# Performance work log

Hardware: AMD Instinct MI355X
Metric: run time of the kernel (lower is better)

Reference implementation:

```python
import jax, jax.numpy as jnp
import numpy as np

PD_THR = 1e-6  # positive-definiteness floor for the diagonal covariance

N_IN, DIM, BATCH = 8192, 128, 4096


def setup_inputs() -> dict:
    key = jax.random.key(0)
    kx, km = jax.random.split(key)
    x = jax.random.normal(kx, (BATCH, DIM), dtype=jnp.float32)
    mean = jax.random.normal(km, (N_IN, DIM), dtype=jnp.float32)
    diag = jnp.ones((N_IN, DIM), dtype=jnp.float32)
    return {"x": x, "mean": mean, "diag": diag}


def reference(x, mean, diag):
    """Energies[b, i] = KL( N(x_b, I) || N(mean_i, diag(diag_i)) ).

    Diagonal-Gaussian KL:
      0.5 * sum_d [ log(diag_id) + (1 + (x_bd - mu_id)^2) / diag_id - 1 ]

    The pairwise quadratic term is expanded into GEMMs to avoid the
    (batch, n_in, dim) broadcast intermediate:
      sum_d (x-mu)^2/diag = x^2 @ inv.T - 2 x @ (mu*inv).T + sum(mu^2*inv)
    Returns (batch, n_in), i.e. the original's energies.T.
    """
    d = jnp.clip(diag, PD_THR, None)              # (n_in, dim)
    inv = 1.0 / d                                 # (n_in, dim)
    # pairwise Mahalanobis quadratic, shape (batch, n_in)
    quad = (
        (x * x) @ inv.T
        - 2.0 * (x @ (mean * inv).T)
        + jnp.sum(mean * mean * inv, axis=-1)     # (n_in,) broadcast
    )
    # per-codebook constants: logdet + trace(inv) - dim
    const = jnp.sum(jnp.log(d), axis=-1) + jnp.sum(inv, axis=-1) - x.shape[-1]
    return 0.5 * (quad + const)                   # (batch, n_in)
```

## Files before the change

### kernel.cpp

```cpp
#include <hip/hip_runtime.h>
#include <hip/hip_bf16.h>


#define BATCH 4096
#define N_IN  8192
#define DIM   128
#define KP    768
#define PD_THR 1e-6f

#define BM 128
#define BN 128
#define BK 64

typedef __attribute__((ext_vector_type(4))) float f32x4;
typedef __attribute__((ext_vector_type(8))) short bf16x8;

static __device__ __forceinline__ unsigned short f2bf(float v) {
    union { __hip_bfloat16 h; unsigned short u; } cv;
    cv.h = __float2bfloat16(v);
    return cv.u;
}
static __device__ __forceinline__ float bf2f(unsigned short u) {
    union { unsigned short u; __hip_bfloat16 h; } cv;
    cv.u = u;
    return __bfloat162float(cv.h);
}

__global__ void prep_a_kernel(const float* __restrict__ x,
                              unsigned short* __restrict__ Ap) {
    int t = blockIdx.x * 256 + threadIdx.x;
    int row = t >> 7;
    int d   = t & 127;
    float v  = x[t];
    float x2 = v * v;
    unsigned short x2h = f2bf(x2);
    unsigned short x2l = f2bf(x2 - bf2f(x2h));
    unsigned short xh  = f2bf(v);
    unsigned short xl  = f2bf(v - bf2f(xh));
    unsigned short* a = Ap + (size_t)row * KP;
    a[d]       = x2h;  a[128 + d] = xh;
    a[256 + d] = x2h;  a[384 + d] = xh;
    a[512 + d] = x2l;  a[640 + d] = xl;
}

__global__ void prep_b_kernel(const float* __restrict__ mean,
                              const float* __restrict__ diag,
                              unsigned short* __restrict__ Bp,
                              float* __restrict__ cvec) {
    int wave = threadIdx.x >> 6, lane = threadIdx.x & 63;
    int row = blockIdx.x * 4 + wave;
    const float* mrow = mean + (size_t)row * DIM;
    const float* drow = diag + (size_t)row * DIM;
    unsigned short* b = Bp + (size_t)row * KP;
    float csum = 0.0f;
#pragma unroll
    for (int j = 0; j < 2; ++j) {
        int d = lane + 64 * j;
        float m   = mrow[d];
        float dd  = fmaxf(drow[d], PD_THR);
        float inv = 1.0f / dd;
        float fm  = -2.0f * m * inv;
        csum += m * m * inv + logf(dd) + inv;
        unsigned short ih = f2bf(inv);
        unsigned short il = f2bf(inv - bf2f(ih));
        unsigned short fh = f2bf(fm);
        unsigned short fl = f2bf(fm - bf2f(fh));
        b[d]       = ih;  b[128 + d] = fh;
        b[256 + d] = il;  b[384 + d] = fl;
        b[512 + d] = ih;  b[640 + d] = fh;
    }
#pragma unroll
    for (int off = 32; off > 0; off >>= 1) csum += __shfl_down(csum, off);
    if (lane == 0) cvec[row] = csum - (float)DIM;
}

__global__ void __launch_bounds__(256)
kl_gemm(const unsigned short* __restrict__ Ap,
        const unsigned short* __restrict__ Bp,
        const float* __restrict__ cvec,
        float* __restrict__ out) {
    __shared__ __align__(16) unsigned short lds_a[BM * BK];
    __shared__ __align__(16) unsigned short lds_b[BM * BK];

    int bid0 = blockIdx.x;
    int bid  = (bid0 & 7) * ((BATCH / BM) * (N_IN / BN) / 8) + (bid0 >> 3);
    int bx = bid & 31;
    int by = bid >> 5;
    int m0 = bx * BM;
    int n0 = by * BN;

    int tid  = threadIdx.x;
    int wave = tid >> 6, lane = tid & 63;
    int wr = wave >> 1, wc = wave & 1;

    f32x4 acc[4][4];
#pragma unroll
    for (int m = 0; m < 4; ++m)
#pragma unroll
        for (int n = 0; n < 4; ++n) acc[m][n] = (f32x4){0.f, 0.f, 0.f, 0.f};

    const int srow = wave * 32 + (lane >> 3);
    const int scol = (lane & 7) * 8;

    for (int k0 = 0; k0 < KP; k0 += BK) {
#pragma unroll
        for (int j = 0; j < 4; ++j) {
            int r = srow + j * 8;
            const unsigned short* ga = Ap + (size_t)(m0 + r) * KP + k0 + scol;
            const unsigned short* gb = Bp + (size_t)(n0 + r) * KP + k0 + scol;
            unsigned short* la = lds_a + (wave * 4 + j) * 512;
            unsigned short* lb = lds_b + (wave * 4 + j) * 512;
            __builtin_amdgcn_global_load_lds(
                (const __attribute__((address_space(1))) void*)ga,
                (__attribute__((address_space(3))) void*)la, 16, 0, 0);
            __builtin_amdgcn_global_load_lds(
                (const __attribute__((address_space(1))) void*)gb,
                (__attribute__((address_space(3))) void*)lb, 16, 0, 0);
        }
        __syncthreads();

#pragma unroll
        for (int kk = 0; kk < BK; kk += 32) {
            bf16x8 af[4], bfr[4];
#pragma unroll
            for (int m = 0; m < 4; ++m)
                af[m] = *(const bf16x8*)&lds_a[(wr * 64 + m * 16 + (lane & 15)) * BK
                                               + kk + (lane >> 4) * 8];
#pragma unroll
            for (int n = 0; n < 4; ++n)
                bfr[n] = *(const bf16x8*)&lds_b[(wc * 64 + n * 16 + (lane & 15)) * BK
                                                + kk + (lane >> 4) * 8];
#pragma unroll
            for (int m = 0; m < 4; ++m)
#pragma unroll
                for (int n = 0; n < 4; ++n)
                    acc[m][n] = __builtin_amdgcn_mfma_f32_16x16x32_bf16(
                        af[m], bfr[n], acc[m][n], 0, 0, 0);
        }
        __syncthreads();
    }

    float* lbw = (float*)lds_a + wave * 1024;
    const int crow0 = m0 + wr * 64;
    const int ccol0 = n0 + wc * 64;
    const int lr = (lane >> 4) << 2;
    const int lc = lane & 15;
#pragma unroll
    for (int m = 0; m < 4; ++m) {
        __syncthreads();
#pragma unroll
        for (int n = 0; n < 4; ++n)
#pragma unroll
            for (int r = 0; r < 4; ++r)
                lbw[(lr + r) * 64 + n * 16 + lc] = acc[m][n][r];
        __syncthreads();
#pragma unroll
        for (int q = 0; q < 4; ++q) {
            int flat = q * 256 + lane * 4;
            int row  = flat >> 6;
            int col  = flat & 63;
            f32x4 v  = *(const f32x4*)&lbw[flat];
            f32x4 c4 = *(const f32x4*)&cvec[ccol0 + col];
            f32x4 o  = (v + c4) * 0.5f;
            __builtin_nontemporal_store(
                o, (f32x4*)&out[(size_t)(crow0 + m * 16 + row) * N_IN + ccol0 + col]);
        }
    }
}

extern "C" void kernel_launch(void* const* d_in, const int* in_sizes, int n_in_args,
                              void* d_out, int out_size, void* d_ws, size_t ws_size,
                              hipStream_t stream) {
    (void)in_sizes; (void)n_in_args; (void)out_size; (void)ws_size;
    const float* x    = (const float*)d_in[0];
    const float* mean = (const float*)d_in[1];
    const float* diag = (const float*)d_in[2];
    float* out = (float*)d_out;

    char* ws = (char*)d_ws;
    unsigned short* Bp = (unsigned short*)ws;
    unsigned short* Ap = (unsigned short*)(ws + (size_t)N_IN * KP * 2);
    float* cvec = (float*)(ws + (size_t)N_IN * KP * 2 + (size_t)BATCH * KP * 2);

    prep_a_kernel<<<BATCH * DIM / 256, 256, 0, stream>>>(x, Ap);
    prep_b_kernel<<<N_IN / 4, 256, 0, stream>>>(mean, diag, Bp, cvec);
    kl_gemm<<<(BATCH / BM) * (N_IN / BN), 256, 0, stream>>>(Ap, Bp, cvec, out);
}
```

Baseline: 223.9 us.

## Enlarge GEMM tiles to 256x256 with double-buffered swizzled LDS pipeline

Grows the block tile to 256x256 with 512 threads (8 waves, each computing 128x64) and double-buffers LDS so global-to-LDS loads for step t+2 overlap the MFMA work on step t. Waits use an explicit vmcnt rather than full syncthreads. LDS rows get an XOR swizzle to avoid bank conflicts, and MFMA sections raise wave priority. The epilogue drops the per-row barriers because each wave writes its own LDS region. In exchange, each wave holds twice as many accumulators, which raises register pressure, and the grid has fewer blocks.

```diff
diff --git a/kernel.cpp b/kernel.cpp
--- a/kernel.cpp
+++ b/kernel.cpp
@@ -8,9 +8,10 @@
 #define KP    768
 #define PD_THR 1e-6f
 
-#define BM 128
-#define BN 128
+#define BM 256
+#define BN 256
 #define BK 64
+#define NT (KP / BK)
 
 typedef __attribute__((ext_vector_type(4))) float f32x4;
 typedef __attribute__((ext_vector_type(8))) short bf16x8;
@@ -74,86 +75,106 @@
     if (lane == 0) cvec[row] = csum - (float)DIM;
 }
 
-__global__ void __launch_bounds__(256)
+__global__ void __launch_bounds__(512, 2)
 kl_gemm(const unsigned short* __restrict__ Ap,
         const unsigned short* __restrict__ Bp,
         const float* __restrict__ cvec,
         float* __restrict__ out) {
-    __shared__ __align__(16) unsigned short lds_a[BM * BK];
-    __shared__ __align__(16) unsigned short lds_b[BM * BK];
+    __shared__ __align__(16) unsigned short lds[2][2 * BM * BK];
 
     int bid0 = blockIdx.x;
-    int bid  = (bid0 & 7) * ((BATCH / BM) * (N_IN / BN) / 8) + (bid0 >> 3);
-    int bx = bid & 31;
-    int by = bid >> 5;
-    int m0 = bx * BM;
-    int n0 = by * BN;
+    int bid  = (bid0 & 7) * 64 + (bid0 >> 3);
+    int bx = bid & 15;
+    int by = bid >> 4;
+    int m0 = bx * BM, n0 = by * BN;
 
     int tid  = threadIdx.x;
     int wave = tid >> 6, lane = tid & 63;
-    int wr = wave >> 1, wc = wave & 1;
-
-    f32x4 acc[4][4];
-#pragma unroll
-    for (int m = 0; m < 4; ++m)
+    int wr = wave >> 2, wc = wave & 3;
+
+    const int lrow  = lane >> 3;
+    const int lslot = (lane & 7) ^ lrow;
+
+    const unsigned short* gA = Ap + (size_t)(m0 + wave * 8 + lrow) * KP + lslot * 8;
+    const unsigned short* gB = Bp + (size_t)(n0 + wave * 8 + lrow) * KP + lslot * 8;
+
+    f32x4 acc[8][4];
+#pragma unroll
+    for (int m = 0; m < 8; ++m)
 #pragma unroll
         for (int n = 0; n < 4; ++n) acc[m][n] = (f32x4){0.f, 0.f, 0.f, 0.f};
 
-    const int srow = wave * 32 + (lane >> 3);
-    const int scol = (lane & 7) * 8;
-
-    for (int k0 = 0; k0 < KP; k0 += BK) {
-#pragma unroll
-        for (int j = 0; j < 4; ++j) {
-            int r = srow + j * 8;
-            const unsigned short* ga = Ap + (size_t)(m0 + r) * KP + k0 + scol;
-            const unsigned short* gb = Bp + (size_t)(n0 + r) * KP + k0 + scol;
-            unsigned short* la = lds_a + (wave * 4 + j) * 512;
-            unsigned short* lb = lds_b + (wave * 4 + j) * 512;
+    auto STAGE = [&](int b, int t) {
+        int k0 = t * BK;
+#pragma unroll
+        for (int j = 0; j < 4; ++j)
             __builtin_amdgcn_global_load_lds(
-                (const __attribute__((address_space(1))) void*)ga,
-                (__attribute__((address_space(3))) void*)la, 16, 0, 0);
+                (const __attribute__((address_space(1))) void*)(gA + (size_t)j * 64 * KP + k0),
+                (__attribute__((address_space(3))) void*)&lds[b][(wave * 8 + j * 64) * 64],
+                16, 0, 0);
+#pragma unroll
+        for (int j = 0; j < 4; ++j)
             __builtin_amdgcn_global_load_lds(
-                (const __attribute__((address_space(1))) void*)gb,
-                (__attribute__((address_space(3))) void*)lb, 16, 0, 0);
-        }
-        __syncthreads();
-
+                (const __attribute__((address_space(1))) void*)(gB + (size_t)j * 64 * KP + k0),
+                (__attribute__((address_space(3))) void*)&lds[b][16384 + (wave * 8 + j * 64) * 64],
+                16, 0, 0);
+    };
+
+    auto COMPUTE = [&](int b) {
+        const unsigned short* La = &lds[b][0];
+        const unsigned short* Lb = &lds[b][16384];
 #pragma unroll
         for (int kk = 0; kk < BK; kk += 32) {
-            bf16x8 af[4], bfr[4];
-#pragma unroll
-            for (int m = 0; m < 4; ++m)
-                af[m] = *(const bf16x8*)&lds_a[(wr * 64 + m * 16 + (lane & 15)) * BK
-                                               + kk + (lane >> 4) * 8];
+            const int phys = (((kk >> 3) + (lane >> 4)) ^ (lane & 7)) * 8;
+            bf16x8 af[8], bf[4];
+#pragma unroll
+            for (int m = 0; m < 8; ++m)
+                af[m] = *(const bf16x8*)&La[(wr * 128 + m * 16 + (lane & 15)) * 64 + phys];
 #pragma unroll
             for (int n = 0; n < 4; ++n)
-                bfr[n] = *(const bf16x8*)&lds_b[(wc * 64 + n * 16 + (lane & 15)) * BK
-                                                + kk + (lane >> 4) * 8];
-#pragma unroll
-            for (int m = 0; m < 4; ++m)
+                bf[n] = *(const bf16x8*)&Lb[(wc * 64 + n * 16 + (lane & 15)) * 64 + phys];
+            __builtin_amdgcn_s_setprio(1);
+#pragma unroll
+            for (int m = 0; m < 8; ++m)
 #pragma unroll
                 for (int n = 0; n < 4; ++n)
                     acc[m][n] = __builtin_amdgcn_mfma_f32_16x16x32_bf16(
-                        af[m], bfr[n], acc[m][n], 0, 0, 0);
+                        af[m], bf[n], acc[m][n], 0, 0, 0);
+            __builtin_amdgcn_s_setprio(0);
         }
-        __syncthreads();
+    };
+
+    STAGE(0, 0);
+    STAGE(1, 1);
+#pragma unroll 1
+    for (int t = 0; t < NT - 1; ++t) {
+        asm volatile("s_waitcnt vmcnt(8)" ::: "memory");
+        __builtin_amdgcn_s_barrier();
+        __builtin_amdgcn_sched_barrier(0);
+        COMPUTE(t & 1);
+        __builtin_amdgcn_s_barrier();
+        __builtin_amdgcn_sched_barrier(0);
+        if (t + 2 < NT) STAGE(t & 1, t + 2);
     }
-
-    float* lbw = (float*)lds_a + wave * 1024;
-    const int crow0 = m0 + wr * 64;
+    asm volatile("s_waitcnt vmcnt(0)" ::: "memory");
+    __builtin_amdgcn_s_barrier();
+    __builtin_amdgcn_sched_barrier(0);
+    COMPUTE((NT - 1) & 1);
+    __builtin_amdgcn_s_barrier();
+    __builtin_amdgcn_sched_barrier(0);
+
+    float* lbw = (float*)&lds[0][0] + wave * 1024;
+    const int crow0 = m0 + wr * 128;
     const int ccol0 = n0 + wc * 64;
     const int lr = (lane >> 4) << 2;
     const int lc = lane & 15;
 #pragma unroll
-    for (int m = 0; m < 4; ++m) {
-        __syncthreads();
+    for (int m = 0; m < 8; ++m) {
 #pragma unroll
         for (int n = 0; n < 4; ++n)
 #pragma unroll
             for (int r = 0; r < 4; ++r)
                 lbw[(lr + r) * 64 + n * 16 + lc] = acc[m][n][r];
-        __syncthreads();
 #pragma unroll
         for (int q = 0; q < 4; ++q) {
             int flat = q * 256 + lane * 4;
@@ -184,5 +205,5 @@
 
     prep_a_kernel<<<BATCH * DIM / 256, 256, 0, stream>>>(x, Ap);
     prep_b_kernel<<<N_IN / 4, 256, 0, stream>>>(mean, diag, Bp, cvec);
-    kl_gemm<<<(BATCH / BM) * (N_IN / BN), 256, 0, stream>>>(Ap, Bp, cvec, out);
-}
+    kl_gemm<<<(BATCH / BM) * (N_IN / BN), 512, 0, stream>>>(Ap, Bp, cvec, out);
+}
```

Measured after the change: 209.5 us. 6.4% less time.
